# Optimization experiments

Hardware: AMD Instinct MI355X
Metric: run time of the kernel (lower is better)

The kernel has to match this reference:

```python
import jax, jax.numpy as jnp
import numpy as np

B, T, N = 512, 64, 30
F_IN, D, C = 512, 256, 7


def setup_inputs() -> dict:
    key = jax.random.key(0)
    ks = jax.random.split(key, 9)
    return {
        "real": jax.random.normal(ks[0], (B, N, F_IN), dtype=jnp.float32),
        "imag": jax.random.normal(ks[1], (B, N, F_IN), dtype=jnp.float32),  # ignored by forward
        "graph_sigs": jax.random.uniform(ks[2], (B, T, N, N), dtype=jnp.float32),
        # DiGCNConv params (glorot-ish weight, zero bias like default init)
        "W": jax.random.normal(ks[3], (F_IN, D), dtype=jnp.float32) / np.sqrt(F_IN),
        "conv_bias": jnp.zeros((D,), dtype=jnp.float32),
        # pool_lin: Linear(D, 1), bias initialized to zero in the module
        "pool_w": jax.random.normal(ks[4], (D,), dtype=jnp.float32) / np.sqrt(D),
        "pool_b": jnp.zeros((), dtype=jnp.float32),
        # head: Conv1d(N, C, kernel_size=1) == dense [C, N] matmul over node scores
        "head_w": jax.random.normal(ks[5], (C, N), dtype=jnp.float32) / np.sqrt(N),
        "head_b": jax.random.normal(ks[6], (C,), dtype=jnp.float32) * 0.01,
    }


def reference(real, imag, graph_sigs, W, conv_bias, pool_w, pool_b, head_w, head_b):
    # Per-graph adjacency: mean over the T signal slices (dominant memory traffic).
    adj = jnp.mean(graph_sigs, axis=1)                      # [B, N, N]
    # DiGCNConv: x @ W, then edge-weighted scatter-add out[dst] += w(src,dst) * xW[src]
    # which for a dense adjacency is exactly adj^T @ xW, plus bias.
    xw = jnp.einsum('bnf,fd->bnd', real, W)                 # [B, N, D]
    agg = jnp.einsum('bij,bid->bjd', adj, xw) + conv_bias   # [B, N, D]
    h = jax.nn.relu(agg)
    # pool_lin -> per-node scalar score
    node_score = jnp.einsum('bnd,d->bn', h, pool_w) + pool_b  # [B, N]
    # Conv1d(N, C, k=1) on [1, N, 1] == node_score @ head_w.T + head_b
    logits = node_score @ head_w.T + head_b                 # [B, C]
    return jax.nn.softmax(logits, axis=-1)
```

## Files before the change

### kernel.cpp

```cpp
#include <hip/hip_runtime.h>

typedef float f32x4 __attribute__((ext_vector_type(4)));

#define B_  512
#define T_  64
#define N_  30
#define FIN 512
#define D_  256
#define C_  7
#define NN  900

__global__ __launch_bounds__(512, 4)
void digcn_fused(const float* __restrict__ real,
                 const float* __restrict__ gs,
                 const float* __restrict__ W,
                 const float* __restrict__ conv_bias,
                 const float* __restrict__ pool_w,
                 const float* __restrict__ pool_b,
                 const float* __restrict__ head_w,
                 const float* __restrict__ head_b,
                 float* __restrict__ out)
{
    __shared__ __align__(16) float xwS[N_ * D_];
    __shared__ __align__(16) float adjS[32 * 32];
    __shared__ float scoreS[4 * 32];
    __shared__ float sumS[32];
    __shared__ float logitS[8];

    const int tid  = threadIdx.x;
    const int b    = blockIdx.x;
    const int w    = tid >> 6;
    const int l    = tid & 63;
    const int kq   = w & 1;
    const int g    = (w >> 1) & 1;
    const int cgrp = w >> 2;
    const int rh   = l >> 5;
    const int r0   = g * 14 + rh * 8;
    const int c0   = cgrp * 128 + (l & 31) * 4;

    const float* realb = real + (size_t)b * (N_ * FIN) + r0 * FIN + kq * 256;
    const float* gsb   = gs   + (size_t)b * (T_ * NN);
    const float* Wb    = W + (size_t)(kq * 256) * D_ + c0;

    f32x4 acc[8];
    #pragma unroll
    for (int rr = 0; rr < 8; ++rr) acc[rr] = (f32x4){0.f, 0.f, 0.f, 0.f};
    float adj0 = 0.f, adj1 = 0.f;

    float pg0 = gsb[tid];
    float pg1 = (tid + 512 < NN) ? gsb[tid + 512] : 0.f;

    for (int it = 0; it < 64; ++it) {
        float ng0 = 0.f, ng1 = 0.f;
        if (it < 63) {
            ng0 = gsb[(it + 1) * NN + tid];
            if (tid + 512 < NN) ng1 = gsb[(it + 1) * NN + tid + 512];
        }
        const float* Wit = Wb + it * 4 * D_;
        f32x4 wv0 = *(const f32x4*)(Wit);
        f32x4 wv1 = *(const f32x4*)(Wit + D_);
        f32x4 wv2 = *(const f32x4*)(Wit + 2 * D_);
        f32x4 wv3 = *(const f32x4*)(Wit + 3 * D_);
        const float* rp = realb + it * 4;
        #pragma unroll
        for (int rr = 0; rr < 8; ++rr) {
            f32x4 rv = *(const f32x4*)(rp + rr * FIN);
            acc[rr] += wv0 * rv[0];
            acc[rr] += wv1 * rv[1];
            acc[rr] += wv2 * rv[2];
            acc[rr] += wv3 * rv[3];
        }
        adj0 += pg0; adj1 += pg1;
        pg0 = ng0;  pg1 = ng1;
    }

    {
        int i = tid / N_, j = tid - i * N_;
        adjS[i * 32 + j] = adj0 * (1.f / (float)T_);
        int e = tid + 512;
        if (e < NN) {
            int i2 = e / N_, j2 = e - i2 * N_;
            adjS[i2 * 32 + j2] = adj1 * (1.f / (float)T_);
        }
        if (tid < 60) adjS[(tid >> 1) * 32 + 30 + (tid & 1)] = 0.f;
    }
    if (kq == 0) {
        #pragma unroll
        for (int rr = 0; rr < 8; ++rr)
            *(f32x4*)(xwS + (r0 + rr) * D_ + c0) = acc[rr];
    }
    __syncthreads();
    if (kq == 1) {
        #pragma unroll
        for (int rr = 0; rr < 8; ++rr) {
            int row = r0 + rr;
            if (!(g == 1 && row < 16)) {
                float* p = xwS + row * D_ + c0;
                *(f32x4*)p = *(const f32x4*)p + acc[rr];
            }
        }
    }
    __syncthreads();

    if (tid < D_) {
        float xcol[N_];
        #pragma unroll
        for (int i = 0; i < N_; ++i) xcol[i] = xwS[i * D_ + tid];
        const float bias = conv_bias[tid];
        const float pw   = pool_w[tid];

        #pragma unroll
        for (int j0 = 0; j0 < N_ + 2; j0 += 4) {
            f32x4 agg = (f32x4){0.f, 0.f, 0.f, 0.f};
            #pragma unroll
            for (int i = 0; i < N_; ++i) {
                f32x4 a4 = *(const f32x4*)(adjS + i * 32 + j0);
                agg += a4 * xcol[i];
            }
            #pragma unroll
            for (int c = 0; c < 4; ++c) {
                if (j0 + c < N_) {
                    float h = agg[c] + bias;
                    h = h > 0.f ? h : 0.f;
                    float v = h * pw;
                    #pragma unroll
                    for (int m = 32; m >= 1; m >>= 1) v += __shfl_xor(v, m, 64);
                    if (l == 0) scoreS[w * 32 + j0 + c] = v;
                }
            }
        }
    }
    __syncthreads();

    if (tid < N_)
        sumS[tid] = scoreS[tid] + scoreS[32 + tid] + scoreS[64 + tid] + scoreS[96 + tid]
                  + pool_b[0];
    __syncthreads();
    if (tid < C_) {
        float lg = head_b[tid];
        #pragma unroll
        for (int j = 0; j < N_; ++j) lg += sumS[j] * head_w[tid * N_ + j];
        logitS[tid] = lg;
    }
    __syncthreads();
    if (tid < C_) {
        float m = logitS[0];
        #pragma unroll
        for (int c = 1; c < C_; ++c) m = fmaxf(m, logitS[c]);
        float s = 0.f;
        #pragma unroll
        for (int c = 0; c < C_; ++c) s += expf(logitS[c] - m);
        out[b * C_ + tid] = expf(logitS[tid] - m) / s;
    }
}

extern "C" void kernel_launch(void* const* d_in, const int* in_sizes, int n_in,
                              void* d_out, int out_size, void* d_ws, size_t ws_size,
                              hipStream_t stream) {
    const float* real      = (const float*)d_in[0];
    const float* gs        = (const float*)d_in[2];
    const float* W         = (const float*)d_in[3];
    const float* conv_bias = (const float*)d_in[4];
    const float* pool_w    = (const float*)d_in[5];
    const float* pool_b    = (const float*)d_in[6];
    const float* head_w    = (const float*)d_in[7];
    const float* head_b    = (const float*)d_in[8];
    float* outp            = (float*)d_out;

    digcn_fused<<<dim3(B_), dim3(512), 0, stream>>>(
        real, gs, W, conv_bias, pool_w, pool_b, head_w, head_b, outp);
}
```

Baseline: 324.2 us.

## Split adjacency mean into separate vectorized pre-kernel via workspace

Moves the mean over the T signal slices out of the fused kernel into a dedicated kernel that reads graph_sigs with 16-byte vector loads across many small blocks and writes a compact [B,N,N] adjacency to workspace. The fused kernel then loads only that adjacency into shared memory and runs the xW matmul without the interleaved scalar graph_sigs loads. The aim is to raise memory-level parallelism on the dominant graph_sigs traffic. In exchange it adds a second launch, a round-trip of the adjacency through global memory, and it serializes the two phases instead of overlapping them.

Measured after the change: 319.1 us. No clear change (-1.6%).

```diff
diff --git a/kernel.cpp b/kernel.cpp
--- a/kernel.cpp
+++ b/kernel.cpp
@@ -10,9 +10,24 @@
 #define C_  7
 #define NN  900
 
+__global__ __launch_bounds__(256)
+void adj_mean(const float* __restrict__ gs, float* __restrict__ adj)
+{
+    const int q  = blockIdx.x * 256 + threadIdx.x;
+    const int b  = q / 225;
+    const int qi = q - b * 225;
+    const float* p = gs + (size_t)b * (T_ * NN) + qi * 4;
+    f32x4 s = (f32x4){0.f, 0.f, 0.f, 0.f};
+    #pragma unroll 8
+    for (int t = 0; t < T_; ++t)
+        s += *(const f32x4*)(p + t * NN);
+    s *= (1.f / (float)T_);
+    *(f32x4*)(adj + (size_t)b * NN + qi * 4) = s;
+}
+
 __global__ __launch_bounds__(512, 4)
 void digcn_fused(const float* __restrict__ real,
-                 const float* __restrict__ gs,
+                 const float* __restrict__ adj,
                  const float* __restrict__ W,
                  const float* __restrict__ conv_bias,
                  const float* __restrict__ pool_w,
@@ -39,23 +54,20 @@
     const int c0   = cgrp * 128 + (l & 31) * 4;
 
     const float* realb = real + (size_t)b * (N_ * FIN) + r0 * FIN + kq * 256;
-    const float* gsb   = gs   + (size_t)b * (T_ * NN);
+    const float* adjb  = adj + (size_t)b * NN;
     const float* Wb    = W + (size_t)(kq * 256) * D_ + c0;
+
+    #pragma unroll
+    for (int e = tid; e < 1024; e += 512) {
+        int i = e >> 5, j = e & 31;
+        adjS[e] = (i < N_ && j < N_) ? adjb[i * N_ + j] : 0.f;
+    }
 
     f32x4 acc[8];
     #pragma unroll
     for (int rr = 0; rr < 8; ++rr) acc[rr] = (f32x4){0.f, 0.f, 0.f, 0.f};
-    float adj0 = 0.f, adj1 = 0.f;
-
-    float pg0 = gsb[tid];
-    float pg1 = (tid + 512 < NN) ? gsb[tid + 512] : 0.f;
 
     for (int it = 0; it < 64; ++it) {
-        float ng0 = 0.f, ng1 = 0.f;
-        if (it < 63) {
-            ng0 = gsb[(it + 1) * NN + tid];
-            if (tid + 512 < NN) ng1 = gsb[(it + 1) * NN + tid + 512];
-        }
         const float* Wit = Wb + it * 4 * D_;
         f32x4 wv0 = *(const f32x4*)(Wit);
         f32x4 wv1 = *(const f32x4*)(Wit + D_);
@@ -70,20 +82,8 @@
             acc[rr] += wv2 * rv[2];
             acc[rr] += wv3 * rv[3];
         }
-        adj0 += pg0; adj1 += pg1;
-        pg0 = ng0;  pg1 = ng1;
     }
 
-    {
-        int i = tid / N_, j = tid - i * N_;
-        adjS[i * 32 + j] = adj0 * (1.f / (float)T_);
-        int e = tid + 512;
-        if (e < NN) {
-            int i2 = e / N_, j2 = e - i2 * N_;
-            adjS[i2 * 32 + j2] = adj1 * (1.f / (float)T_);
-        }
-        if (tid < 60) adjS[(tid >> 1) * 32 + 30 + (tid & 1)] = 0.f;
-    }
     if (kq == 0) {
         #pragma unroll
         for (int rr = 0; rr < 8; ++rr)
@@ -166,7 +166,9 @@
     const float* head_w    = (const float*)d_in[7];
     const float* head_b    = (const float*)d_in[8];
     float* outp            = (float*)d_out;
+    float* adjw            = (float*)d_ws;
 
+    adj_mean<<<dim3(450), dim3(256), 0, stream>>>(gs, adjw);
     digcn_fused<<<dim3(B_), dim3(512), 0, stream>>>(
-        real, gs, W, conv_bias, pool_w, pool_b, head_w, head_b, outp);
+        real, adjw, W, conv_bias, pool_w, pool_b, head_w, head_b, outp);
 }
```
